# Optimization experiments

Hardware: AMD Instinct MI355X
Metric: run time of the kernel (lower is better)

Reference implementation:

```python
import jax, jax.numpy as jnp
import numpy as np

BIT = 4  # layer_bits
QMAX = 2 ** (BIT - 1) - 1  # 7


def setup_inputs() -> dict:
    key = jax.random.key(0)
    k_in, k_qw, k_fw, k_a, k_b, k_n, k_out = jax.random.split(key, 7)
    in_features, out_features, outlier_num = 8192, 8192, 256
    q_in = in_features - outlier_num  # 7936
    tokens = 64

    inp = jax.random.normal(k_in, (tokens, in_features), dtype=jnp.float32)
    q_w = jax.random.normal(k_qw, (out_features, q_in), dtype=jnp.float32)
    fp_w = jax.random.normal(k_fw, (out_features, outlier_num), dtype=jnp.float32)
    # alpha_scale: positive per-row clip scale (init ones in torch; use ~U(0.5,1.5))
    alpha = jax.random.uniform(k_a, (out_features, 1), dtype=jnp.float32) + 0.5
    bias = jax.random.normal(k_b, (out_features,), dtype=jnp.float32)
    noise = jax.random.normal(k_n, (out_features, q_in), dtype=jnp.float32)

    # build col_perm / inv_col_perm from a deterministic set of outlier column ids
    rng = np.random.RandomState(0)
    outlier_ids = rng.choice(in_features, size=outlier_num, replace=False)
    mask = np.ones(in_features, dtype=bool)
    mask[outlier_ids] = False
    col_ids = np.arange(in_features, dtype=np.int32)
    col_perm = np.concatenate([col_ids[mask], col_ids[~mask]])
    inv_col_perm = np.zeros_like(col_perm)
    inv_col_perm[col_perm] = np.arange(in_features, dtype=np.int32)

    return {
        "input": inp,
        "sasut_q_weight": q_w,
        "sasut_fp_weight": fp_w,
        "alpha_scale": alpha,
        "bias": bias,
        "noise": noise,
        "inv_col_perm": jnp.asarray(inv_col_perm),
    }


def reference(input, sasut_q_weight, sasut_fp_weight, alpha_scale, bias, noise, inv_col_perm):
    # BitNoiseQuant._compute_quant_noise, training path with trainable alpha:
    # delta = alpha / qmax ; normal noise -> randn/2
    w = sasut_q_weight
    delta = alpha_scale / QMAX                       # [out, 1]
    w_rand = (noise * 0.5) * delta                   # [out, q_in]
    w_noised = jnp.where(
        w >= alpha_scale,
        alpha_scale,
        jnp.where(w <= -alpha_scale, -alpha_scale, w + w_rand),
    )
    # hstack quantized + fp outlier blocks, then undo the column permutation
    out_w = jnp.concatenate([w_noised, sasut_fp_weight], axis=1)  # [out, in]
    out_w = out_w[:, inv_col_perm]
    # F.linear: input @ out_w.T + bias
    return input @ out_w.T + bias
```

## Files before the change

kernel.cpp:

```cpp
#include <hip/hip_runtime.h>

#define TOK    64
#define NOUT   8192
#define KTOT   8192
#define KQ     7936
#define KFP    256
#define KSPLIT 2
#define KBLK   (KTOT / KSPLIT)
#define BK     128
#define NS     (KBLK / BK)

typedef float f32x4 __attribute__((ext_vector_type(4)));
typedef short s16x8 __attribute__((ext_vector_type(8)));

__device__ __forceinline__ unsigned short f2bf(float f) {
    unsigned int u = __float_as_uint(f);
    u += 0x7fffu + ((u >> 16) & 1u);
    return (unsigned short)(u >> 16);
}

__device__ __forceinline__ void gload_lds16(const void* g, void* l) {
    __builtin_amdgcn_global_load_lds(
        (const __attribute__((address_space(1))) void*)g,
        (__attribute__((address_space(3))) void*)l, 16, 0, 0);
}

__global__ void prep(const float* __restrict__ inp, const int* __restrict__ invp,
                     const float* __restrict__ bias,
                     unsigned short* __restrict__ xp, float* __restrict__ out) {
    int idx = blockIdx.x * blockDim.x + threadIdx.x;
    int j = idx & (KTOT - 1);
    xp[(idx >> 13) * KTOT + invp[j]] = f2bf(inp[idx]);
    out[idx] = bias[j];
}

__global__ __launch_bounds__(512) void sasut_gemm(
    const unsigned short* __restrict__ xp,
    const float* __restrict__ qw,
    const float* __restrict__ fpw,
    const float* __restrict__ alpha,
    const float* __restrict__ noise,
    float* __restrict__ out)
{
    __shared__ __attribute__((aligned(16))) char smem[2 * 16384];
    const int tid  = threadIdx.x;
    const int w    = tid >> 6;
    const int lane = tid & 63;
    const int nloc = lane & 15;
    const int quad = lane >> 4;
    const int mt   = w & 3;
    const int h    = w >> 2;
    const int ct   = blockIdx.x & 511;
    const int sp   = blockIdx.x >> 9;
    const int nbase = ct * 16;
    const int koff  = sp * KBLK;

    const float a_s  = alpha[nbase + nloc];
    const float c_s  = a_s * (1.0f / 14.0f);
    const float na_s = -a_s;

    const int sr = 2 * w + (lane >> 5);
    const int gc = (lane & 31) ^ (sr & 7);
    const size_t qrow_off = (size_t)(nbase + sr) * KQ + gc * 4;
    const size_t frow_off = (size_t)(nbase + sr) * KFP + gc * 4;

    const int sw = nloc & 7;

    const unsigned short* xrow =
        xp + (size_t)(mt * 16 + nloc) * KTOT + koff + h * 64 + quad * 8;

    auto stage = [&](int s, int buf) {
        const int kb = koff + s * BK;
        char* ldq = smem + buf * 16384 + w * 1024;
        if (kb < KQ) {
            gload_lds16(qw + qrow_off + kb, ldq);
            gload_lds16(noise + qrow_off + kb, ldq + 8192);
        } else {
            gload_lds16(fpw + frow_off + (kb - KQ), ldq);
        }
    };

    f32x4 acc = {0.f, 0.f, 0.f, 0.f};

    stage(0, 0);
    s16x8 af0 = *(const s16x8*)(xrow);
    s16x8 af1 = *(const s16x8*)(xrow + 32);
    __syncthreads();

    #pragma unroll 2
    for (int s = 0; s < NS; ++s) {
        const int nxt = s + 1;
        s16x8 nf0 = af0, nf1 = af1;
        if (nxt < NS) {
            stage(nxt, nxt & 1);
            nf0 = *(const s16x8*)(xrow + nxt * BK);
            nf1 = *(const s16x8*)(xrow + nxt * BK + 32);
        }
        const float* qb_ = (const float*)(smem + (s & 1) * 16384) + nloc * 128;
        const float* nb_ = qb_ + 2048;
        const bool isfp = (koff + s * BK) >= KQ;
        #pragma unroll
        for (int i = 0; i < 2; ++i) {
            const int kt = h * 64 + i * 32;
            const int c0 = (kt >> 2) + quad * 2;
            f32x4 qa = *(const f32x4*)(qb_ + ((c0 ^ sw) << 2));
            f32x4 qc = *(const f32x4*)(qb_ + (((c0 + 1) ^ sw) << 2));
            s16x8 bf;
            if (!isfp) {
                f32x4 na = *(const f32x4*)(nb_ + ((c0 ^ sw) << 2));
                f32x4 nc = *(const f32x4*)(nb_ + (((c0 + 1) ^ sw) << 2));
                #pragma unroll
                for (int j = 0; j < 8; ++j) {
                    float wv = (j < 4) ? qa[j] : qc[j - 4];
                    float nz = (j < 4) ? na[j] : nc[j - 4];
                    float t = fmaf(nz, c_s, wv);
                    t = (wv >= a_s)  ? a_s  : t;
                    t = (wv <= na_s) ? na_s : t;
                    bf[j] = (short)f2bf(t);
                }
            } else {
                #pragma unroll
                for (int j = 0; j < 8; ++j) {
                    float wv = (j < 4) ? qa[j] : qc[j - 4];
                    bf[j] = (short)f2bf(wv);
                }
            }
            acc = __builtin_amdgcn_mfma_f32_16x16x32_bf16(
                (i == 0) ? af0 : af1, bf, acc, 0, 0, 0);
        }
        __syncthreads();
        af0 = nf0; af1 = nf1;
    }

    float* red = (float*)smem;
    #pragma unroll
    for (int r = 0; r < 4; ++r)
        red[(w * 16 + quad * 4 + r) * 17 + nloc] = acc[r];
    __syncthreads();
    #pragma unroll
    for (int rep = 0; rep < 2; ++rep) {
        int e   = tid + rep * 512;
        int m   = e >> 8;
        int tl  = (e >> 4) & 15;
        int col = e & 15;
        float v = red[(m * 16 + tl) * 17 + col] +
                  red[((m + 4) * 16 + tl) * 17 + col];
        atomicAdd(out + (size_t)(m * 16 + tl) * NOUT + nbase + col, v);
    }
}

extern "C" void kernel_launch(void* const* d_in, const int* in_sizes, int n_in,
                              void* d_out, int out_size, void* d_ws, size_t ws_size,
                              hipStream_t stream) {
    const float* inp   = (const float*)d_in[0];
    const float* qw    = (const float*)d_in[1];
    const float* fpw   = (const float*)d_in[2];
    const float* alpha = (const float*)d_in[3];
    const float* bias  = (const float*)d_in[4];
    const float* noise = (const float*)d_in[5];
    const int*   invp  = (const int*)d_in[6];
    float* out = (float*)d_out;
    unsigned short* xp = (unsigned short*)d_ws;

    prep<<<(TOK * KTOT) / 256, 256, 0, stream>>>(inp, invp, bias, xp, out);
    sasut_gemm<<<512 * KSPLIT, 512, 0, stream>>>(xp, qw, fpw, alpha, noise, out);
}
```

Before: 539.9 us.

## Split K across waves in-block, drop split-K atomics and LDS staging

Each block now owns 16 output columns over the full K range. Its 8 waves each take a contiguous K chunk, load weights and noise straight from global memory into registers, and reuse each dequantized B fragment across four MFMAs, one per 16-token tile. This removes the global-to-LDS staging, the per-step barriers, the cross-block split-K atomics and the bias pre-initialization, and bias is added in the final in-block reduction. In exchange the weight loads are no longer staged or prefetched, so latency hiding depends on occupancy and the 2x unroll, and there are half as many blocks.

New measurement: 549.4 us. No clear change (+1.8%).

```diff
diff --git a/kernel.cpp b/kernel.cpp
--- a/kernel.cpp
+++ b/kernel.cpp
@@ -5,10 +5,9 @@
 #define KTOT   8192
 #define KQ     7936
 #define KFP    256
-#define KSPLIT 2
-#define KBLK   (KTOT / KSPLIT)
-#define BK     128
-#define NS     (KBLK / BK)
+#define NWAVE  8
+#define WCH    (KTOT / NWAVE)
+#define NS     (WCH / 32)
 
 typedef float f32x4 __attribute__((ext_vector_type(4)));
 typedef short s16x8 __attribute__((ext_vector_type(8)));
@@ -19,123 +18,93 @@
     return (unsigned short)(u >> 16);
 }
 
-__device__ __forceinline__ void gload_lds16(const void* g, void* l) {
-    __builtin_amdgcn_global_load_lds(
-        (const __attribute__((address_space(1))) void*)g,
-        (__attribute__((address_space(3))) void*)l, 16, 0, 0);
-}
-
 __global__ void prep(const float* __restrict__ inp, const int* __restrict__ invp,
-                     const float* __restrict__ bias,
-                     unsigned short* __restrict__ xp, float* __restrict__ out) {
+                     unsigned short* __restrict__ xp) {
     int idx = blockIdx.x * blockDim.x + threadIdx.x;
     int j = idx & (KTOT - 1);
     xp[(idx >> 13) * KTOT + invp[j]] = f2bf(inp[idx]);
-    out[idx] = bias[j];
 }
 
-__global__ __launch_bounds__(512) void sasut_gemm(
+__global__ __launch_bounds__(512, 4) void sasut_gemm(
     const unsigned short* __restrict__ xp,
     const float* __restrict__ qw,
     const float* __restrict__ fpw,
     const float* __restrict__ alpha,
     const float* __restrict__ noise,
+    const float* __restrict__ bias,
     float* __restrict__ out)
 {
-    __shared__ __attribute__((aligned(16))) char smem[2 * 16384];
+    __shared__ float red[NWAVE][4][16][17];
     const int tid  = threadIdx.x;
     const int w    = tid >> 6;
     const int lane = tid & 63;
     const int nloc = lane & 15;
     const int quad = lane >> 4;
-    const int mt   = w & 3;
-    const int h    = w >> 2;
-    const int ct   = blockIdx.x & 511;
-    const int sp   = blockIdx.x >> 9;
-    const int nbase = ct * 16;
-    const int koff  = sp * KBLK;
+    const int nbase = blockIdx.x * 16;
+    const int kw   = w * WCH;
 
-    const float a_s  = alpha[nbase + nloc];
+    const int row = nbase + nloc;
+    const float a_s  = alpha[row];
     const float c_s  = a_s * (1.0f / 14.0f);
     const float na_s = -a_s;
 
-    const int sr = 2 * w + (lane >> 5);
-    const int gc = (lane & 31) ^ (sr & 7);
-    const size_t qrow_off = (size_t)(nbase + sr) * KQ + gc * 4;
-    const size_t frow_off = (size_t)(nbase + sr) * KFP + gc * 4;
+    const float* qp  = qw    + (size_t)row * KQ  + kw + quad * 8;
+    const float* np  = noise + (size_t)row * KQ  + kw + quad * 8;
+    const float* fpq = fpw   + (size_t)row * KFP + quad * 8;
 
-    const int sw = nloc & 7;
+    const unsigned short* x0 = xp + (size_t)nloc * KTOT + kw + quad * 8;
+    const unsigned short* x1 = x0 + (size_t)16 * KTOT;
+    const unsigned short* x2 = x0 + (size_t)32 * KTOT;
+    const unsigned short* x3 = x0 + (size_t)48 * KTOT;
 
-    const unsigned short* xrow =
-        xp + (size_t)(mt * 16 + nloc) * KTOT + koff + h * 64 + quad * 8;
-
-    auto stage = [&](int s, int buf) {
-        const int kb = koff + s * BK;
-        char* ldq = smem + buf * 16384 + w * 1024;
-        if (kb < KQ) {
-            gload_lds16(qw + qrow_off + kb, ldq);
-            gload_lds16(noise + qrow_off + kb, ldq + 8192);
-        } else {
-            gload_lds16(fpw + frow_off + (kb - KQ), ldq);
-        }
-    };
-
-    f32x4 acc = {0.f, 0.f, 0.f, 0.f};
-
-    stage(0, 0);
-    s16x8 af0 = *(const s16x8*)(xrow);
-    s16x8 af1 = *(const s16x8*)(xrow + 32);
-    __syncthreads();
+    f32x4 acc0 = {0.f, 0.f, 0.f, 0.f};
+    f32x4 acc1 = acc0, acc2 = acc0, acc3 = acc0;
 
     #pragma unroll 2
     for (int s = 0; s < NS; ++s) {
-        const int nxt = s + 1;
-        s16x8 nf0 = af0, nf1 = af1;
-        if (nxt < NS) {
-            stage(nxt, nxt & 1);
-            nf0 = *(const s16x8*)(xrow + nxt * BK);
-            nf1 = *(const s16x8*)(xrow + nxt * BK + 32);
+        const int k_ = kw + s * 32;
+        s16x8 a0f = *(const s16x8*)(x0 + s * 32);
+        s16x8 a1f = *(const s16x8*)(x1 + s * 32);
+        s16x8 a2f = *(const s16x8*)(x2 + s * 32);
+        s16x8 a3f = *(const s16x8*)(x3 + s * 32);
+        s16x8 bf;
+        if (k_ < KQ) {
+            f32x4 qa = *(const f32x4*)(qp + s * 32);
+            f32x4 qc = *(const f32x4*)(qp + s * 32 + 4);
+            f32x4 na = *(const f32x4*)(np + s * 32);
+            f32x4 nc = *(const f32x4*)(np + s * 32 + 4);
+            #pragma unroll
+            for (int j = 0; j < 8; ++j) {
+                float wv = (j < 4) ? qa[j] : qc[j - 4];
+                float nz = (j < 4) ? na[j] : nc[j - 4];
+                float t = fmaf(nz, c_s, wv);
+                t = (wv >= a_s)  ? a_s  : t;
+                t = (wv <= na_s) ? na_s : t;
+                bf[j] = (short)f2bf(t);
+            }
+        } else {
+            const float* f_ = fpq + (k_ - KQ);
+            f32x4 qa = *(const f32x4*)(f_);
+            f32x4 qc = *(const f32x4*)(f_ + 4);
+            #pragma unroll
+            for (int j = 0; j < 8; ++j) {
+                float wv = (j < 4) ? qa[j] : qc[j - 4];
+                bf[j] = (short)f2bf(wv);
+            }
         }
-        const float* qb_ = (const float*)(smem + (s & 1) * 16384) + nloc * 128;
-        const float* nb_ = qb_ + 2048;
-        const bool isfp = (koff + s * BK) >= KQ;
-        #pragma unroll
-        for (int i = 0; i < 2; ++i) {
-            const int kt = h * 64 + i * 32;
-            const int c0 = (kt >> 2) + quad * 2;
-            f32x4 qa = *(const f32x4*)(qb_ + ((c0 ^ sw) << 2));
-            f32x4 qc = *(const f32x4*)(qb_ + (((c0 + 1) ^ sw) << 2));
-            s16x8 bf;
-            if (!isfp) {
-                f32x4 na = *(const f32x4*)(nb_ + ((c0 ^ sw) << 2));
-                f32x4 nc = *(const f32x4*)(nb_ + (((c0 + 1) ^ sw) << 2));
-                #pragma unroll
-                for (int j = 0; j < 8; ++j) {
-                    float wv = (j < 4) ? qa[j] : qc[j - 4];
-                    float nz = (j < 4) ? na[j] : nc[j - 4];
-                    float t = fmaf(nz, c_s, wv);
-                    t = (wv >= a_s)  ? a_s  : t;
-                    t = (wv <= na_s) ? na_s : t;
-                    bf[j] = (short)f2bf(t);
-                }
-            } else {
-                #pragma unroll
-                for (int j = 0; j < 8; ++j) {
-                    float wv = (j < 4) ? qa[j] : qc[j - 4];
-                    bf[j] = (short)f2bf(wv);
-                }
-            }
-            acc = __builtin_amdgcn_mfma_f32_16x16x32_bf16(
-                (i == 0) ? af0 : af1, bf, acc, 0, 0, 0);
-        }
-        __syncthreads();
-        af0 = nf0; af1 = nf1;
+        acc0 = __builtin_amdgcn_mfma_f32_16x16x32_bf16(a0f, bf, acc0, 0, 0, 0);
+        acc1 = __builtin_amdgcn_mfma_f32_16x16x32_bf16(a1f, bf, acc1, 0, 0, 0);
+        acc2 = __builtin_amdgcn_mfma_f32_16x16x32_bf16(a2f, bf, acc2, 0, 0, 0);
+        acc3 = __builtin_amdgcn_mfma_f32_16x16x32_bf16(a3f, bf, acc3, 0, 0, 0);
     }
 
-    float* red = (float*)smem;
     #pragma unroll
-    for (int r = 0; r < 4; ++r)
-        red[(w * 16 + quad * 4 + r) * 17 + nloc] = acc[r];
+    for (int r = 0; r < 4; ++r) {
+        red[w][0][quad * 4 + r][nloc] = acc0[r];
+        red[w][1][quad * 4 + r][nloc] = acc1[r];
+        red[w][2][quad * 4 + r][nloc] = acc2[r];
+        red[w][3][quad * 4 + r][nloc] = acc3[r];
+    }
     __syncthreads();
     #pragma unroll
     for (int rep = 0; rep < 2; ++rep) {
@@ -143,9 +112,10 @@
         int m   = e >> 8;
         int tl  = (e >> 4) & 15;
         int col = e & 15;
-        float v = red[(m * 16 + tl) * 17 + col] +
-                  red[((m + 4) * 16 + tl) * 17 + col];
-        atomicAdd(out + (size_t)(m * 16 + tl) * NOUT + nbase + col, v);
+        float v = bias[nbase + col];
+        #pragma unroll
+        for (int ww = 0; ww < NWAVE; ++ww) v += red[ww][m][tl][col];
+        out[(size_t)(m * 16 + tl) * NOUT + nbase + col] = v;
     }
 }
 
@@ -162,6 +132,6 @@
     float* out = (float*)d_out;
     unsigned short* xp = (unsigned short*)d_ws;
 
-    prep<<<(TOK * KTOT) / 256, 256, 0, stream>>>(inp, invp, bias, xp, out);
-    sasut_gemm<<<512 * KSPLIT, 512, 0, stream>>>(xp, qw, fpw, alpha, noise, out);
+    prep<<<(TOK * KTOT) / 256, 256, 0, stream>>>(inp, invp, xp);
+    sasut_gemm<<<512, 512, 0, stream>>>(xp, qw, fpw, alpha, noise, bias, out);
 }
```
